# Kernel optimization log

Measured on AMD Instinct MI355X. Metric: run time of the kernel, lower is better.

## Reference

```python
import jax, jax.numpy as jnp
import numpy as np

EPSILON = 0.1
ITERATIONS = 100
THRESHOLD = 0.1


def setup_inputs() -> dict:
    key = jax.random.key(0)
    kx, ky = jax.random.split(key)
    x = jax.random.normal(kx, (2048, 64), dtype=jnp.float32)
    y = jax.random.normal(ky, (2048, 64), dtype=jnp.float32)
    return {"x": x, "y": y}


def _sinkhorn(x, y):
    N, M = x.shape[0], y.shape[0]
    # l2 ground metric: C[i,j] = sum_d (x[i,d] - y[j,d])^2   -> [N, M]
    C = jnp.sum((x[:, None, :] - y[None, :, :]) ** 2, axis=-1)
    log_a = jnp.log(1.0 / N + 1e-8)  # uniform marginals (scalar broadcast)
    log_b = jnp.log(1.0 / M + 1e-8)

    def kernel(u, v):
        # log Boltzmann kernel: (-C + u_i + v_j) / epsilon
        return (-C + u[:, None] + v[None, :]) / EPSILON

    def step(carry, _):
        u, v, done = carry
        K = kernel(u, v)
        u_new = EPSILON * (log_a - jax.nn.logsumexp(K, axis=1)) + u
        K2 = kernel(u_new, v)
        # torch: logsumexp(K2.T, dim=1) == logsumexp(K2, axis=0)
        v_new = EPSILON * (log_b - jax.nn.logsumexp(K2, axis=0)) + v
        diff = jnp.sum(jnp.abs(u_new - u)) + jnp.sum(jnp.abs(v_new - v))
        # emulate the host-side early break: freeze state once converged
        u_out = jnp.where(done, u, u_new)
        v_out = jnp.where(done, v, v_new)
        done = done | (diff < THRESHOLD)
        return (u_out, v_out, done), None

    init = (jnp.zeros((N,), C.dtype), jnp.zeros((M,), C.dtype),
            jnp.asarray(False))
    (u, v, _), _ = jax.lax.scan(step, init, None, length=ITERATIONS)

    pi = jnp.exp(kernel(u, v))          # transport plan [N, M]
    cost = jnp.sum(pi * C)              # scalar OT cost
    return cost, pi


def reference(x, y):
    return _sinkhorn(x, y)
```

## Files before the change

kernel.cpp:

```cpp
#include <hip/hip_runtime.h>
#include <cstddef>

static constexpr int   NN      = 2048;
static constexpr int   TPB_B   = 256;
static constexpr int   TPB     = 1024;
static constexpr int   NWB     = TPB / 64;
static constexpr int   NB      = 128;
static constexpr int   MAX_IT  = 100;
static constexpr float EPS     = 0.1f;
static constexpr float INV_EPS = 10.0f;
static constexpr float LOG_AB  = -7.6245985063594f;
static constexpr float THRESH  = 0.1f;

#define ALOAD(p)     __hip_atomic_load((p),  __ATOMIC_RELAXED, __HIP_MEMORY_SCOPE_AGENT)
#define ASTORE(p, x) __hip_atomic_store((p), (x), __ATOMIC_RELAXED, __HIP_MEMORY_SCOPE_AGENT)

typedef unsigned long long u64;

__global__ __launch_bounds__(TPB_B)
void build_cost(const float* __restrict__ x, const float* __restrict__ y,
                float* __restrict__ C, float* __restrict__ CT,
                unsigned* __restrict__ zz, int zcount,
                int c_aligned, int use_ct)
{
    __shared__ float xs[64][65];
    __shared__ float ys[64][65];
    const int t  = threadIdx.x;
    const int bi = blockIdx.y, bj = blockIdx.x;

    if (bi == 0) {
        int per = (zcount + 31) / 32;
        int lo = bj * per;
        int hi = lo + per; if (hi > zcount) hi = zcount;
        for (int idx = lo + t; idx < hi; idx += TPB_B) zz[idx] = 0u;
    }

#pragma unroll
    for (int k = 0; k < 16; ++k) {
        int idx = t + TPB_B * k;
        int r = idx >> 6, c = idx & 63;
        xs[r][c] = x[(size_t)(bi * 64 + r) * 64 + c];
        ys[r][c] = y[(size_t)(bj * 64 + r) * 64 + c];
    }
    __syncthreads();

    const int ti0 = (t >> 4) * 4;
    const int tj0 = (t & 15) * 4;
    float acc[4][4] = {};
#pragma unroll 8
    for (int d = 0; d < 64; ++d) {
        float xv[4], yv[4];
#pragma unroll
        for (int k = 0; k < 4; ++k) xv[k] = xs[ti0 + k][d];
#pragma unroll
        for (int l = 0; l < 4; ++l) yv[l] = ys[tj0 + l][d];
#pragma unroll
        for (int k = 0; k < 4; ++k)
#pragma unroll
            for (int l = 0; l < 4; ++l) {
                float df = xv[k] - yv[l];
                acc[k][l] = fmaf(df, df, acc[k][l]);
            }
    }

#pragma unroll
    for (int k = 0; k < 4; ++k) {
        size_t off = (size_t)(bi * 64 + ti0 + k) * NN + bj * 64 + tj0;
        if (c_aligned) {
            *(float4*)(C + off) = make_float4(acc[k][0], acc[k][1], acc[k][2], acc[k][3]);
        } else {
            C[off + 0] = acc[k][0]; C[off + 1] = acc[k][1];
            C[off + 2] = acc[k][2]; C[off + 3] = acc[k][3];
        }
    }
    if (use_ct) {
#pragma unroll
        for (int l = 0; l < 4; ++l) {
            size_t off = (size_t)(bj * 64 + tj0 + l) * NN + bi * 64 + ti0;
            *(float4*)(CT + off) = make_float4(acc[0][l], acc[1][l], acc[2][l], acc[3][l]);
        }
    }
}

__device__ __forceinline__ void load_row32(const float* row, int lane,
                                           int aligned, float c[32])
{
    if (aligned) {
        const float4* r4 = (const float4*)row;
#pragma unroll
        for (int k = 0; k < 8; ++k) {
            float4 A = r4[lane + 64 * k];
            c[4*k+0] = A.x; c[4*k+1] = A.y; c[4*k+2] = A.z; c[4*k+3] = A.w;
        }
    } else {
#pragma unroll
        for (int k = 0; k < 8; ++k) {
            const float* p = row + 4 * (lane + 64 * k);
            c[4*k+0] = p[0]; c[4*k+1] = p[1]; c[4*k+2] = p[2]; c[4*k+3] = p[3];
        }
    }
}

__device__ __forceinline__ void lds_row32(const float* sv, int lane, float b[32])
{
    const float4* s4 = (const float4*)sv;
#pragma unroll
    for (int k = 0; k < 8; ++k) {
        float4 A = s4[lane + 64 * k];
        b[4*k+0] = A.x; b[4*k+1] = A.y; b[4*k+2] = A.z; b[4*k+3] = A.w;
    }
}

__device__ __forceinline__ float wave_lse(const float c[32], const float b[32])
{
    float M = b[0] - c[0];
#pragma unroll
    for (int k = 1; k < 32; ++k) M = fmaxf(M, b[k] - c[k]);
#pragma unroll
    for (int off = 1; off < 64; off <<= 1) M = fmaxf(M, __shfl_xor(M, off));
    float Ms = M * INV_EPS;
    float s = 0.0f;
#pragma unroll
    for (int k = 0; k < 32; ++k) s += __expf(fmaf(b[k] - c[k], INV_EPS, -Ms));
#pragma unroll
    for (int off = 1; off < 64; off <<= 1) s += __shfl_xor(s, off);
    return Ms + __logf(s);
}

__global__ __launch_bounds__(TPB)
void sinkhorn_main(const float* Cm, const float* __restrict__ CT,
                   u64* __restrict__ valA, u64* __restrict__ valB,
                   u64* __restrict__ rotR, u64* __restrict__ rotC,
                   u64* __restrict__ costb,
                   float* out, int c_aligned, int use_ct)
{
    __shared__ float sv[2048];
    __shared__ float swave[NWB];
    __shared__ float sdw[NWB];
    __shared__ float sred4[4];
    __shared__ float sdiff;
    const int t = threadIdx.x, lane = t & 63, w = t >> 6, b = blockIdx.x;
    const int i = b * NWB + w;

    float crow[32], ccol[32];
    load_row32(Cm + (size_t)i * NN, lane, c_aligned, crow);
    if (use_ct) {
        load_row32(CT + (size_t)i * NN, lane, 1, ccol);
    } else {
#pragma unroll
        for (int k = 0; k < 8; ++k)
#pragma unroll
            for (int kk = 0; kk < 4; ++kk)
                ccol[4*k+kk] = Cm[(size_t)(4 * (lane + 64 * k) + kk) * NN + i];
    }

    for (int k = t; k < 2048; k += TPB) sv[k] = 0.0f;
    __syncthreads();

    float u_keep = 0.0f, v_keep = 0.0f;
    float b32[32];

    for (int it = 0; it < MAX_IT; ++it) {
        const unsigned ep = (unsigned)(it + 1);

        lds_row32(sv, lane, b32);
        float lse   = wave_lse(crow, b32);
        float u_new = EPS * (LOG_AB - lse);
        float pdr   = fabsf(u_new - u_keep);

        if (it >= 1) {
            if (t < NB) {
                u64 r1, r2;
                const int ri = (it & 3) * NB + t;
                for (;;) { r1 = ALOAD(&rotR[ri]);
                           if ((unsigned)(r1 >> 32) >= (unsigned)it) break; }
                for (;;) { r2 = ALOAD(&rotC[ri]);
                           if ((unsigned)(r2 >> 32) >= (unsigned)it) break; }
                float d = __uint_as_float((unsigned)r1) +
                          __uint_as_float((unsigned)r2);
#pragma unroll
                for (int off = 1; off < 64; off <<= 1) d += __shfl_xor(d, off);
                if (lane == 0) sred4[w] = d;
            }
            __syncthreads();
            if (t == 0) sdiff = sred4[0] + sred4[1];
            __syncthreads();
            if (sdiff < THRESH) break;
        }
        u_keep = u_new;

        if (lane == 0) { swave[w] = u_new; sdw[w] = pdr; }
        __syncthreads();
        if (t < NWB)
            ASTORE(&valA[b * NWB + t],
                   ((u64)ep << 32) | __float_as_uint(swave[t]));
        if (t == 0) {
            float ps = 0.0f;
#pragma unroll
            for (int k = 0; k < NWB; ++k) ps += sdw[k];
            ASTORE(&rotR[(ep & 3) * NB + b],
                   ((u64)ep << 32) | __float_as_uint(ps));
        }
        {
            const int base = 2 * t;
            u64 d0, d1;
            for (;;) {
                d0 = ALOAD(&valA[base + 0]);
                d1 = ALOAD(&valA[base + 1]);
                if (((unsigned)(d0 >> 32) >= ep) & ((unsigned)(d1 >> 32) >= ep))
                    break;
            }
            ((float2*)sv)[t] = make_float2(__uint_as_float((unsigned)d0),
                                           __uint_as_float((unsigned)d1));
        }
        __syncthreads();

        lds_row32(sv, lane, b32);
        lse = wave_lse(ccol, b32);
        float v_new = EPS * (LOG_AB - lse);
        float pdc   = fabsf(v_new - v_keep);
        v_keep = v_new;

        if (lane == 0) { swave[w] = v_new; sdw[w] = pdc; }
        __syncthreads();
        if (t < NWB)
            ASTORE(&valB[b * NWB + t],
                   ((u64)ep << 32) | __float_as_uint(swave[t]));
        if (t == 0) {
            float ps = 0.0f;
#pragma unroll
            for (int k = 0; k < NWB; ++k) ps += sdw[k];
            ASTORE(&rotC[(ep & 3) * NB + b],
                   ((u64)ep << 32) | __float_as_uint(ps));
        }
        {
            const int base = 2 * t;
            u64 d0, d1;
            for (;;) {
                d0 = ALOAD(&valB[base + 0]);
                d1 = ALOAD(&valB[base + 1]);
                if (((unsigned)(d0 >> 32) >= ep) & ((unsigned)(d1 >> 32) >= ep))
                    break;
            }
            ((float2*)sv)[t] = make_float2(__uint_as_float((unsigned)d0),
                                           __uint_as_float((unsigned)d1));
        }
        __syncthreads();
    }

    float cpart = 0.0f;
    {
        lds_row32(sv, lane, b32);
        const float ui = u_keep;
        float* orow = out + 1 + (size_t)i * NN;
#pragma unroll
        for (int k = 0; k < 8; ++k) {
#pragma unroll
            for (int kk = 0; kk < 4; ++kk) {
                float cc = crow[4*k+kk];
                float p  = __expf((ui + b32[4*k+kk] - cc) * INV_EPS);
                cpart = fmaf(p, cc, cpart);
                orow[4 * (lane + 64 * k) + kk] = p;
            }
        }
    }
#pragma unroll
    for (int off = 1; off < 64; off <<= 1) cpart += __shfl_xor(cpart, off);
    if (lane == 0) sdw[w] = cpart;
    __syncthreads();
    if (t == 0) {
        float pc = 0.0f;
#pragma unroll
        for (int k = 0; k < NWB; ++k) pc += sdw[k];
        ASTORE(&costb[b], (1ull << 32) | __float_as_uint(pc));
    }
    if (b == 0) {
        if (t < NB) {
            u64 h;
            for (;;) { h = ALOAD(&costb[t]); if (h >= (1ull << 32)) break; }
            float pc = __uint_as_float((unsigned)h);
#pragma unroll
            for (int off = 1; off < 64; off <<= 1) pc += __shfl_xor(pc, off);
            if (lane == 0) sred4[w] = pc;
        }
        __syncthreads();
        if (t == 0) out[0] = sred4[0] + sred4[1];
    }
}

extern "C" void kernel_launch(void* const* d_in, const int* in_sizes, int n_in,
                              void* d_out, int out_size, void* d_ws, size_t ws_size,
                              hipStream_t stream)
{
    (void)in_sizes; (void)n_in; (void)out_size;
    const float* x = (const float*)d_in[0];
    const float* y = (const float*)d_in[1];
    float* out = (float*)d_out;
    char*  ws  = (char*)d_ws;

    const size_t CB = (size_t)NN * NN * sizeof(float);
    const int    ZU = 2048 + 2048 + 512 + 512 + 128;
    const size_t ZB = (size_t)ZU * sizeof(u64);

    float *Cm, *CT; char* zz;
    int c_aligned, use_ct;
    if (ws_size >= 2 * CB + ZB) {
        Cm = (float*)ws; CT = (float*)(ws + CB); zz = ws + 2 * CB;
        c_aligned = 1; use_ct = 1;
    } else if (ws_size >= CB + ZB) {
        Cm = out + 1; CT = (float*)ws; zz = ws + CB;
        c_aligned = 0; use_ct = 1;
    } else {
        Cm = out + 1; CT = nullptr; zz = ws;
        c_aligned = 0; use_ct = 0;
    }
    u64* valA  = (u64*)zz;
    u64* valB  = valA + 2048;
    u64* rotR  = valB + 2048;
    u64* rotC  = rotR + 512;
    u64* costb = rotC + 512;
    int  zcount = ZU * 2;

    hipLaunchKernelGGL(build_cost, dim3(32, 32), dim3(TPB_B), 0, stream,
                       x, y, Cm, CT, (unsigned*)zz, zcount, c_aligned, use_ct);

    const float* Cmc = Cm;
    const float* CTc = CT;
    void* args[] = { (void*)&Cmc, (void*)&CTc, (void*)&valA, (void*)&valB,
                     (void*)&rotR, (void*)&rotC, (void*)&costb,
                     (void*)&out, (void*)&c_aligned, (void*)&use_ct };
    hipLaunchCooperativeKernel((void*)sinkhorn_main, dim3(NB), dim3(TPB),
                               args, 0, stream);
}
```

Baseline: 737.6 us.

## Publish row potentials before convergence check and stagger cross-block polling

Each block now writes its new u values and its row-diff partial to global memory before it waits on the previous iteration's convergence reduction, so the exchange overlaps with the diff check. The spin-wait that gathers all blocks' values becomes a helper that stops reloading entries already seen as ready. Each block starts polling at a different offset to spread contention on the shared flag arrays. The extra publish happens even on the iteration that breaks, which is harmless because every block leaves the loop on the same iteration.

```diff
diff --git a/kernel.cpp b/kernel.cpp
--- a/kernel.cpp
+++ b/kernel.cpp
@@ -127,6 +127,21 @@
     return Ms + __logf(s);
 }
 
+__device__ __forceinline__ void poll_dep(const u64* __restrict__ arr, unsigned ep,
+                                         float* sv, int p)
+{
+    const int base = 2 * p;
+    u64 d0 = 0, d1 = 0;
+    bool k0 = false, k1 = false;
+    for (;;) {
+        if (!k0) { d0 = ALOAD(&arr[base + 0]); k0 = ((unsigned)(d0 >> 32) >= ep); }
+        if (!k1) { d1 = ALOAD(&arr[base + 1]); k1 = ((unsigned)(d1 >> 32) >= ep); }
+        if (k0 & k1) break;
+    }
+    ((float2*)sv)[p] = make_float2(__uint_as_float((unsigned)d0),
+                                   __uint_as_float((unsigned)d1));
+}
+
 __global__ __launch_bounds__(TPB)
 void sinkhorn_main(const float* Cm, const float* __restrict__ CT,
                    u64* __restrict__ valA, u64* __restrict__ valB,
@@ -141,6 +156,7 @@
     __shared__ float sdiff;
     const int t = threadIdx.x, lane = t & 63, w = t >> 6, b = blockIdx.x;
     const int i = b * NWB + w;
+    const int p = (t + b * 64) & (TPB - 1);
 
     float crow[32], ccol[32];
     load_row32(Cm + (size_t)i * NN, lane, c_aligned, crow);
@@ -167,6 +183,19 @@
         float lse   = wave_lse(crow, b32);
         float u_new = EPS * (LOG_AB - lse);
         float pdr   = fabsf(u_new - u_keep);
+
+        if (lane == 0) { swave[w] = u_new; sdw[w] = pdr; }
+        __syncthreads();
+        if (t < NWB)
+            ASTORE(&valA[b * NWB + t],
+                   ((u64)ep << 32) | __float_as_uint(swave[t]));
+        if (t == 0) {
+            float ps = 0.0f;
+#pragma unroll
+            for (int k = 0; k < NWB; ++k) ps += sdw[k];
+            ASTORE(&rotR[(ep & 3) * NB + b],
+                   ((u64)ep << 32) | __float_as_uint(ps));
+        }
 
         if (it >= 1) {
             if (t < NB) {
@@ -189,30 +218,7 @@
         }
         u_keep = u_new;
 
-        if (lane == 0) { swave[w] = u_new; sdw[w] = pdr; }
-        __syncthreads();
-        if (t < NWB)
-            ASTORE(&valA[b * NWB + t],
-                   ((u64)ep << 32) | __float_as_uint(swave[t]));
-        if (t == 0) {
-            float ps = 0.0f;
-#pragma unroll
-            for (int k = 0; k < NWB; ++k) ps += sdw[k];
-            ASTORE(&rotR[(ep & 3) * NB + b],
-                   ((u64)ep << 32) | __float_as_uint(ps));
-        }
-        {
-            const int base = 2 * t;
-            u64 d0, d1;
-            for (;;) {
-                d0 = ALOAD(&valA[base + 0]);
-                d1 = ALOAD(&valA[base + 1]);
-                if (((unsigned)(d0 >> 32) >= ep) & ((unsigned)(d1 >> 32) >= ep))
-                    break;
-            }
-            ((float2*)sv)[t] = make_float2(__uint_as_float((unsigned)d0),
-                                           __uint_as_float((unsigned)d1));
-        }
+        poll_dep(valA, ep, sv, p);
         __syncthreads();
 
         lds_row32(sv, lane, b32);
@@ -233,18 +239,7 @@
             ASTORE(&rotC[(ep & 3) * NB + b],
                    ((u64)ep << 32) | __float_as_uint(ps));
         }
-        {
-            const int base = 2 * t;
-            u64 d0, d1;
-            for (;;) {
-                d0 = ALOAD(&valB[base + 0]);
-                d1 = ALOAD(&valB[base + 1]);
-                if (((unsigned)(d0 >> 32) >= ep) & ((unsigned)(d1 >> 32) >= ep))
-                    break;
-            }
-            ((float2*)sv)[t] = make_float2(__uint_as_float((unsigned)d0),
-                                           __uint_as_float((unsigned)d1));
-        }
+        poll_dep(valB, ep, sv, p);
         __syncthreads();
     }
 
@@ -258,9 +253,9 @@
 #pragma unroll
             for (int kk = 0; kk < 4; ++kk) {
                 float cc = crow[4*k+kk];
-                float p  = __expf((ui + b32[4*k+kk] - cc) * INV_EPS);
-                cpart = fmaf(p, cc, cpart);
-                orow[4 * (lane + 64 * k) + kk] = p;
+                float p2 = __expf((ui + b32[4*k+kk] - cc) * INV_EPS);
+                cpart = fmaf(p2, cc, cpart);
+                orow[4 * (lane + 64 * k) + kk] = p2;
             }
         }
     }
```

New measurement: 780.6 us. 5.8% more time.
